# Kernel tuning notes

Hardware: AMD Instinct MI355X
Metric: run time of the kernel (lower is better)

## Reference

```python
import jax, jax.numpy as jnp
import numpy as np

D_IN = 768
D_OUT = 768
N_HEADS = 12
HEAD_DIM = D_OUT // N_HEADS


def setup_inputs() -> dict:
    key = jax.random.key(0)
    ks = jax.random.split(key, 6)
    B, S = 2, 4096
    x = jax.random.normal(ks[0], (B, S, D_IN), dtype=jnp.float32)
    s = 0.02
    Wq = jax.random.normal(ks[1], (D_IN, D_OUT), dtype=jnp.float32) * s
    Wk = jax.random.normal(ks[2], (D_IN, D_OUT), dtype=jnp.float32) * s
    Wv = jax.random.normal(ks[3], (D_IN, D_OUT), dtype=jnp.float32) * s
    Wo = jax.random.normal(ks[4], (D_OUT, D_OUT), dtype=jnp.float32) * s
    bo = jnp.zeros((D_OUT,), dtype=jnp.float32)
    return {"x": x, "Wq": Wq, "Wk": Wk, "Wv": Wv, "Wo": Wo, "bo": bo}


def reference(x, Wq, Wk, Wv, Wo, bo):
    B, S, _ = x.shape
    # QKV projections (no bias), reshape to [B, H, S, Dh]
    q = (x @ Wq).reshape(B, S, N_HEADS, HEAD_DIM).transpose(0, 2, 1, 3)
    k = (x @ Wk).reshape(B, S, N_HEADS, HEAD_DIM).transpose(0, 2, 1, 3)
    v = (x @ Wv).reshape(B, S, N_HEADS, HEAD_DIM).transpose(0, 2, 1, 3)
    # scores: [B, H, S, S], causal mask, scaled softmax
    scores = jnp.einsum('bhqd,bhkd->bhqk', q, k)
    causal = jnp.triu(jnp.ones((S, S), dtype=bool), k=1)
    scores = jnp.where(causal, -jnp.inf, scores)
    attn = jax.nn.softmax(scores / np.sqrt(HEAD_DIM).astype(np.float32), axis=-1)
    # dropout p=0.0 -> identity
    ctx = jnp.einsum('bhqk,bhkd->bqhd', attn, v).reshape(B, S, D_OUT)
    return ctx @ Wo + bo
```

## Files before the change

### kernel.cpp

```cpp
#include <hip/hip_runtime.h>

#define S 4096
#define BATCH 2
#define D 768
#define NH 12
#define DH 64
#define NROWS (BATCH * S)
#define N_ITEMS (32 * NH * BATCH)
#define CTR_OFF 67633152

typedef __attribute__((ext_vector_type(8))) short bf16x8;
typedef __attribute__((ext_vector_type(4))) float f32x4;
typedef __attribute__((ext_vector_type(2))) unsigned uint32x2;

__device__ __forceinline__ unsigned short f2bf(float f) {
    unsigned u = __builtin_bit_cast(unsigned, f);
    u += 0x7fff + ((u >> 16) & 1);
    return (unsigned short)(u >> 16);
}

__device__ __forceinline__ float fexp2(float x) {
#if __has_builtin(__builtin_amdgcn_exp2f)
    return __builtin_amdgcn_exp2f(x);
#else
    return exp2f(x);
#endif
}

#define GLDS16(g, l)                                                   \
    __builtin_amdgcn_global_load_lds(                                  \
        (const __attribute__((address_space(1))) void*)(g),            \
        (__attribute__((address_space(3))) void*)(l), 16, 0, 0)

__global__ __launch_bounds__(256) void cvt_x(const float* __restrict__ x,
                                             unsigned short* __restrict__ xb)
{
    int i = (blockIdx.x * 256 + threadIdx.x) * 4;
    float4 v = *(const float4*)(x + i);
    ushort4 o = make_ushort4(f2bf(v.x), f2bf(v.y), f2bf(v.z), f2bf(v.w));
    *(ushort4*)(xb + i) = o;
}

__global__ __launch_bounds__(256) void cvt_w(
    const float* __restrict__ Wq, const float* __restrict__ Wk,
    const float* __restrict__ Wv, const float* __restrict__ Wo,
    unsigned short* __restrict__ wt)
{
    __shared__ float tile[32][33];
    const int z = blockIdx.z;
    const float* W = (z == 0) ? Wq : (z == 1) ? Wk : (z == 2) ? Wv : Wo;
    const int k0 = blockIdx.x * 32, n0 = blockIdx.y * 32;
    const int t = threadIdx.x;
    const int r = t >> 3, c4 = (t & 7) * 4;

    float4 v = *(const float4*)(W + (size_t)(k0 + r) * D + n0 + c4);
    tile[r][c4 + 0] = v.x; tile[r][c4 + 1] = v.y;
    tile[r][c4 + 2] = v.z; tile[r][c4 + 3] = v.w;
    __syncthreads();
    ushort4 o = make_ushort4(f2bf(tile[c4 + 0][r]), f2bf(tile[c4 + 1][r]),
                             f2bf(tile[c4 + 2][r]), f2bf(tile[c4 + 3][r]));
    *(ushort4*)(wt + ((size_t)z * D + n0 + r) * D + k0 + c4) = o;
}

__global__ __launch_bounds__(256) void gemm_qkv(
    const unsigned short* __restrict__ xb,
    const unsigned short* __restrict__ wt,
    unsigned short* __restrict__ qb, unsigned short* __restrict__ kb,
    unsigned short* __restrict__ vtb)
{
    __shared__ unsigned short As[128 * 64];
    __shared__ unsigned short Bs[128 * 64];

    const int t = threadIdx.x;
    const int lane = t & 63, w = t >> 6;
    const int l16 = lane & 15, quad = lane >> 4;
    const int wm = w & 1, wn = w >> 1;
    const int m0 = blockIdx.x * 128;
    const int n0g = blockIdx.y * 128;
    const int z = n0g / 768;
    const int c0 = n0g - z * 768;
    const unsigned short* Wz = wt + (size_t)z * D * D;

    f32x4 acc[4][4] = {};

    for (int k0 = 0; k0 < D; k0 += 64) {
#pragma unroll
        for (int i = 0; i < 4; ++i) {
            int g = i * 256 + w * 64 + lane;
            int row = g >> 3, cl = g & 7, cg = cl ^ (row & 7);
            GLDS16(xb + (size_t)(m0 + row) * D + k0 + cg * 8,
                   As + (size_t)(i * 256 + w * 64) * 8);
            GLDS16(Wz + (size_t)(c0 + row) * D + k0 + cg * 8,
                   Bs + (size_t)(i * 256 + w * 64) * 8);
        }
        __syncthreads();
#pragma unroll
        for (int kk = 0; kk < 2; ++kk) {
            bf16x8 af[4], bf_[4];
#pragma unroll
            for (int mt = 0; mt < 4; ++mt) {
                int r = wm * 64 + mt * 16 + l16;
                int c = kk * 4 + quad;
                af[mt] = *(const bf16x8*)&As[(r * 8 + (c ^ (r & 7))) * 8];
            }
#pragma unroll
            for (int nt = 0; nt < 4; ++nt) {
                int r = wn * 64 + nt * 16 + l16;
                int c = kk * 4 + quad;
                bf_[nt] = *(const bf16x8*)&Bs[(r * 8 + (c ^ (r & 7))) * 8];
            }
#pragma unroll
            for (int mt = 0; mt < 4; ++mt)
#pragma unroll
                for (int nt = 0; nt < 4; ++nt)
                    acc[mt][nt] = __builtin_amdgcn_mfma_f32_16x16x32_bf16(
                        af[mt], bf_[nt], acc[mt][nt], 0, 0, 0);
        }
        __syncthreads();
    }

    if (z < 2) {
        unsigned short* outp = (z == 0) ? qb : kb;
        const float scale = (z == 0) ? 0.18033688011112042f : 1.0f;
#pragma unroll
        for (int mt = 0; mt < 4; ++mt) {
#pragma unroll
            for (int reg = 0; reg < 4; ++reg) {
                int m = wm * 64 + mt * 16 + quad * 4 + reg;
                int ng = m0 + m;
                int b = ng >> 12, s = ng & 4095;
#pragma unroll
                for (int nt = 0; nt < 4; ++nt) {
                    int n = c0 + wn * 64 + nt * 16 + l16;
                    int h = n >> 6, dh = n & 63;
                    outp[(((size_t)b * NH + h) * S + s) * DH + dh] =
                        f2bf(acc[mt][nt][reg] * scale);
                }
            }
        }
    } else {
#pragma unroll
        for (int mt = 0; mt < 4; ++mt) {
#pragma unroll
            for (int nt = 0; nt < 4; ++nt) {
                int m = wm * 64 + mt * 16 + quad * 4;
                int ng = m0 + m;
                int b = ng >> 12, s = ng & 4095;
                int n = c0 + wn * 64 + nt * 16 + l16;
                int h = n >> 6, dh = n & 63;
                ushort4 p = make_ushort4(
                    f2bf(acc[mt][nt][0]), f2bf(acc[mt][nt][1]),
                    f2bf(acc[mt][nt][2]), f2bf(acc[mt][nt][3]));
                *(ushort4*)(vtb + (((size_t)b * NH + h) * DH + dh) * S + s) = p;
            }
        }
    }
}

__global__ __launch_bounds__(256, 3) void attn_mfma(
    const unsigned short* __restrict__ qg,
    const unsigned short* __restrict__ kg,
    const unsigned short* __restrict__ vtg,
    unsigned short* __restrict__ ctxb,
    int* __restrict__ work_ctr)
{
    __shared__ unsigned short Ks[2][64 * 64];
    __shared__ unsigned short Vs[2][64 * 64];
    __shared__ int s_item;

    const float INF = __builtin_inff();
    const int t = threadIdx.x;
    const int w = t >> 6, lane = t & 63;
    const int l16 = lane & 15, quad = lane >> 4;
    const int a7 = l16 & 7;
    const int sg = w * 64 + lane;

    bf16x8 vone;
#pragma unroll
    for (int i = 0; i < 8; ++i) vone[i] = (short)0x3F80;

    for (;;) {
        if (t == 0) s_item = atomicAdd(work_ctr, 1);
        __syncthreads();
        const int p = s_item;
        if (p >= N_ITEMS) return;

        const int qt = 31 - (p / (NH * BATCH));
        const int hb = p % (NH * BATCH);
        const int h = hb % NH, b = hb / NH;
        const size_t hbase = ((size_t)b * NH + h) * (size_t)S * DH;
        const unsigned short* kp = kg + hbase;
        const unsigned short* vp = vtg + hbase;

        bf16x8 bq[2][2];
#pragma unroll
        for (int qs = 0; qs < 2; ++qs) {
            int qrow = qt * 128 + w * 32 + qs * 16 + l16;
#pragma unroll
            for (int kk = 0; kk < 2; ++kk)
                bq[qs][kk] = *(const bf16x8*)(qg + hbase + (size_t)qrow * DH +
                                              kk * 32 + quad * 8);
        }

        f32x4 acc_o[2][4] = {};
        f32x4 acc_sum[2] = {};

        const int jmax = 2 * qt + 1, jd = 2 * qt;

#pragma unroll
        for (int i = 0; i < 2; ++i) {
            int g = i * 256 + sg;
            int row = g >> 3, cl = g & 7, cg = cl ^ (row & 7);
            GLDS16(kp + (size_t)row * DH + cg * 8,
                   &Ks[0][(size_t)(i * 256 + w * 64) * 8]);
            GLDS16(vp + (size_t)row * S + cg * 8,
                   &Vs[0][(size_t)(i * 256 + w * 64) * 8]);
        }

        for (int j = 0; j <= jmax; ++j) {
            const int cur = j & 1;
            __syncthreads();
            if (j < jmax) {
#pragma unroll
                for (int i = 0; i < 2; ++i) {
                    int g = i * 256 + sg;
                    int row = g >> 3, cl = g & 7, cg = cl ^ (row & 7);
                    GLDS16(kp + (size_t)((j + 1) * 64 + row) * DH + cg * 8,
                           &Ks[cur ^ 1][(size_t)(i * 256 + w * 64) * 8]);
                    GLDS16(vp + (size_t)row * S + (j + 1) * 64 + cg * 8,
                           &Vs[cur ^ 1][(size_t)(i * 256 + w * 64) * 8]);
                }
            }

            const unsigned short* Kc = Ks[cur];
            const unsigned short* Vc = Vs[cur];

            f32x4 acc_s[2][4] = {};
            __builtin_amdgcn_s_setprio(1);
#pragma unroll
            for (int kk = 0; kk < 2; ++kk)
#pragma unroll
                for (int ms = 0; ms < 4; ++ms) {
                    int r = ms * 16 + l16, c = kk * 4 + quad;
                    bf16x8 ak = *(const bf16x8*)&Kc[(r * 8 + (c ^ a7)) * 8];
#pragma unroll
                    for (int qs = 0; qs < 2; ++qs)
                        acc_s[qs][ms] = __builtin_amdgcn_mfma_f32_16x16x32_bf16(
                            ak, bq[qs][kk], acc_s[qs][ms], 0, 0, 0);
                }
            __builtin_amdgcn_s_setprio(0);

            if (j >= jd) {
#pragma unroll
                for (int qs = 0; qs < 2; ++qs) {
                    int qrow_g = qt * 128 + w * 32 + qs * 16 + l16;
#pragma unroll
                    for (int ms = 0; ms < 4; ++ms)
#pragma unroll
                        for (int reg = 0; reg < 4; ++reg)
                            if ((j * 64 + ms * 16 + quad * 4 + reg) > qrow_g)
                                acc_s[qs][ms][reg] = -INF;
                }
            }

            bf16x8 bp[2][2];
#pragma unroll
            for (int qs = 0; qs < 2; ++qs) {
                unsigned ulo[4], uhi[4];
#pragma unroll
                for (int ms = 0; ms < 4; ++ms) {
                    float e0 = fexp2(acc_s[qs][ms][0]);
                    float e1 = fexp2(acc_s[qs][ms][1]);
                    float e2 = fexp2(acc_s[qs][ms][2]);
                    float e3 = fexp2(acc_s[qs][ms][3]);
                    asm("v_cvt_pk_bf16_f32 %0, %1, %2"
                        : "=v"(ulo[ms]) : "v"(e0), "v"(e1));
                    asm("v_cvt_pk_bf16_f32 %0, %1, %2"
                        : "=v"(uhi[ms]) : "v"(e2), "v"(e3));
                }
#pragma unroll
                for (int kp2 = 0; kp2 < 2; ++kp2) {
                    uint32x2 lo = __builtin_amdgcn_permlane32_swap(
                        ulo[2 * kp2], ulo[2 * kp2 + 1], false, false);
                    uint32x2 s02 = __builtin_amdgcn_permlane16_swap(
                        lo[0], lo[1], false, false);
                    uint32x2 hi = __builtin_amdgcn_permlane32_swap(
                        uhi[2 * kp2], uhi[2 * kp2 + 1], false, false);
                    uint32x2 s13 = __builtin_amdgcn_permlane16_swap(
                        hi[0], hi[1], false, false);
                    union { unsigned u[4]; bf16x8 v; } pb;
                    pb.u[0] = s02[0]; pb.u[1] = s13[0];
                    pb.u[2] = s02[1]; pb.u[3] = s13[1];
                    bp[qs][kp2] = pb.v;
                }
            }

            __builtin_amdgcn_s_setprio(1);
#pragma unroll
            for (int kk = 0; kk < 2; ++kk) {
#pragma unroll
                for (int d = 0; d < 4; ++d) {
                    int r = d * 16 + l16, c = kk * 4 + quad;
                    bf16x8 av = *(const bf16x8*)&Vc[(r * 8 + (c ^ a7)) * 8];
#pragma unroll
                    for (int qs = 0; qs < 2; ++qs)
                        acc_o[qs][d] = __builtin_amdgcn_mfma_f32_16x16x32_bf16(
                            av, bp[qs][kk], acc_o[qs][d], 0, 0, 0);
                }
#pragma unroll
                for (int qs = 0; qs < 2; ++qs)
                    acc_sum[qs] = __builtin_amdgcn_mfma_f32_16x16x32_bf16(
                        vone, bp[qs][kk], acc_sum[qs], 0, 0, 0);
            }
            __builtin_amdgcn_s_setprio(0);
        }

#pragma unroll
        for (int qs = 0; qs < 2; ++qs) {
            float inv = 1.f / acc_sum[qs][0];
            int qrow = qt * 128 + w * 32 + qs * 16 + l16;
            size_t base = ((size_t)(b * S + qrow)) * D + h * 64;
#pragma unroll
            for (int d = 0; d < 4; ++d) {
                ushort4 o;
                o.x = f2bf(acc_o[qs][d][0] * inv);
                o.y = f2bf(acc_o[qs][d][1] * inv);
                o.z = f2bf(acc_o[qs][d][2] * inv);
                o.w = f2bf(acc_o[qs][d][3] * inv);
                *(ushort4*)(ctxb + base + d * 16 + quad * 4) = o;
            }
        }
    }
}

__global__ __launch_bounds__(256) void gemm_out(
    const unsigned short* __restrict__ ctxb,
    const unsigned short* __restrict__ wt,
    const float* __restrict__ bo,
    float* __restrict__ out)
{
    __shared__ unsigned short As[128 * 64];
    __shared__ unsigned short Bs[128 * 64];

    const int t = threadIdx.x;
    const int lane = t & 63, w = t >> 6;
    const int l16 = lane & 15, quad = lane >> 4;
    const int wm = w & 1, wn = w >> 1;
    const int m0 = blockIdx.x * 128;
    const int n0 = blockIdx.y * 128;
    const unsigned short* Wz = wt + (size_t)3 * D * D;

    f32x4 acc[4][4] = {};

    for (int k0 = 0; k0 < D; k0 += 64) {
#pragma unroll
        for (int i = 0; i < 4; ++i) {
            int g = i * 256 + w * 64 + lane;
            int row = g >> 3, cl = g & 7, cg = cl ^ (row & 7);
            GLDS16(ctxb + (size_t)(m0 + row) * D + k0 + cg * 8,
                   As + (size_t)(i * 256 + w * 64) * 8);
            GLDS16(Wz + (size_t)(n0 + row) * D + k0 + cg * 8,
                   Bs + (size_t)(i * 256 + w * 64) * 8);
        }
        __syncthreads();
#pragma unroll
        for (int kk = 0; kk < 2; ++kk) {
            bf16x8 af[4], bf_[4];
#pragma unroll
            for (int mt = 0; mt < 4; ++mt) {
                int r = wm * 64 + mt * 16 + l16;
                int c = kk * 4 + quad;
                af[mt] = *(const bf16x8*)&As[(r * 8 + (c ^ (r & 7))) * 8];
            }
#pragma unroll
            for (int nt = 0; nt < 4; ++nt) {
                int r = wn * 64 + nt * 16 + l16;
                int c = kk * 4 + quad;
                bf_[nt] = *(const bf16x8*)&Bs[(r * 8 + (c ^ (r & 7))) * 8];
            }
#pragma unroll
            for (int mt = 0; mt < 4; ++mt)
#pragma unroll
                for (int nt = 0; nt < 4; ++nt)
                    acc[mt][nt] = __builtin_amdgcn_mfma_f32_16x16x32_bf16(
                        af[mt], bf_[nt], acc[mt][nt], 0, 0, 0);
        }
        __syncthreads();
    }

    float bv[4];
#pragma unroll
    for (int nt = 0; nt < 4; ++nt)
        bv[nt] = bo[n0 + wn * 64 + nt * 16 + l16];
#pragma unroll
    for (int mt = 0; mt < 4; ++mt)
#pragma unroll
        for (int reg = 0; reg < 4; ++reg) {
            int m = m0 + wm * 64 + mt * 16 + quad * 4 + reg;
#pragma unroll
            for (int nt = 0; nt < 4; ++nt)
                out[(size_t)m * D + n0 + wn * 64 + nt * 16 + l16] =
                    acc[mt][nt][reg] + bv[nt];
        }
}

extern "C" void kernel_launch(void* const* d_in, const int* in_sizes, int n_in,
                              void* d_out, int out_size, void* d_ws, size_t ws_size,
                              hipStream_t stream)
{
    const float* x  = (const float*)d_in[0];
    const float* Wq = (const float*)d_in[1];
    const float* Wk = (const float*)d_in[2];
    const float* Wv = (const float*)d_in[3];
    const float* Wo = (const float*)d_in[4];
    const float* bo = (const float*)d_in[5];
    float* out = (float*)d_out;

    const size_t elems = (size_t)NROWS * D;
    unsigned short* xb   = (unsigned short*)d_ws;
    unsigned short* wt   = xb + elems;
    unsigned short* q    = wt + (size_t)4 * D * D;
    unsigned short* k    = q + elems;
    unsigned short* vt   = k + elems;
    unsigned short* ctxb = vt + elems;
    int* work_ctr = (int*)((char*)d_ws + CTR_OFF);

    hipMemsetAsync(work_ctr, 0, sizeof(int), stream);

    cvt_x<<<NROWS * D / 1024, 256, 0, stream>>>(x, xb);
    dim3 gw(D / 32, D / 32, 4);
    cvt_w<<<gw, 256, 0, stream>>>(Wq, Wk, Wv, Wo, wt);

    dim3 g1(NROWS / 128, (3 * D) / 128);
    gemm_qkv<<<g1, 256, 0, stream>>>(xb, wt, q, k, vt);

    attn_mfma<<<512, 256, 0, stream>>>(q, k, vt, ctxb, work_ctr);

    dim3 g3(NROWS / 128, D / 128);
    gemm_out<<<g3, 256, 0, stream>>>(ctxb, wt, bo, out);
}
```

Baseline: 238.3 us.

## Software-pipeline QK^T of next tile with softmax/PV of current tile

```diff
diff --git a/kernel.cpp b/kernel.cpp
--- a/kernel.cpp
+++ b/kernel.cpp
@@ -157,6 +157,120 @@
     }
 }
 
+#define QK_CLUSTER(KSRC, DST)                                                \
+    {                                                                        \
+        _Pragma("unroll")                                                    \
+        for (int qs = 0; qs < 2; ++qs)                                       \
+            _Pragma("unroll")                                                \
+            for (int ms = 0; ms < 4; ++ms)                                   \
+                DST[qs][ms] = zf4;                                           \
+        __builtin_amdgcn_s_setprio(1);                                       \
+        _Pragma("unroll")                                                    \
+        for (int kk = 0; kk < 2; ++kk)                                       \
+            _Pragma("unroll")                                                \
+            for (int ms = 0; ms < 4; ++ms) {                                 \
+                int r = ms * 16 + l16, c = kk * 4 + quad;                    \
+                bf16x8 ak = *(const bf16x8*)&(KSRC)[(r * 8 + (c ^ a7)) * 8]; \
+                _Pragma("unroll")                                            \
+                for (int qs = 0; qs < 2; ++qs)                               \
+                    DST[qs][ms] = __builtin_amdgcn_mfma_f32_16x16x32_bf16(   \
+                        ak, bq[qs][kk], DST[qs][ms], 0, 0, 0);               \
+            }                                                                \
+        __builtin_amdgcn_s_setprio(0);                                       \
+    }
+
+#define PIPE_BODY(J, PAR, CUR, NXT)                                          \
+    {                                                                        \
+        const int j_ = (J);                                                  \
+        __builtin_amdgcn_sched_barrier(0);                                   \
+        __syncthreads();                                                     \
+        __builtin_amdgcn_sched_barrier(0);                                   \
+        if (j_ + 2 <= jmax) {                                                \
+            _Pragma("unroll")                                                \
+            for (int i = 0; i < 2; ++i) {                                    \
+                int g = i * 256 + sg;                                        \
+                int row = g >> 3, cg = (g & 7) ^ (row & 7);                  \
+                GLDS16(kp + (size_t)((j_ + 2) * 64 + row) * DH + cg * 8,     \
+                       &Ks[PAR][(size_t)(i * 256 + w * 64) * 8]);            \
+            }                                                                \
+        }                                                                    \
+        if (j_ + 1 <= jmax) {                                                \
+            _Pragma("unroll")                                                \
+            for (int i = 0; i < 2; ++i) {                                    \
+                int g = i * 256 + sg;                                        \
+                int row = g >> 3, cg = (g & 7) ^ (row & 7);                  \
+                GLDS16(vp + (size_t)row * S + (j_ + 1) * 64 + cg * 8,        \
+                       &Vs[(PAR) ^ 1][(size_t)(i * 256 + w * 64) * 8]);      \
+            }                                                                \
+        }                                                                    \
+        __builtin_amdgcn_sched_barrier(0);                                   \
+        if (j_ + 1 <= jmax) {                                                \
+            QK_CLUSTER(Ks[(PAR) ^ 1], NXT)                                   \
+        }                                                                    \
+        if (j_ >= jd) {                                                      \
+            _Pragma("unroll")                                                \
+            for (int qs = 0; qs < 2; ++qs) {                                 \
+                int qrow_g = qt * 128 + w * 32 + qs * 16 + l16;              \
+                _Pragma("unroll")                                            \
+                for (int ms = 0; ms < 4; ++ms)                               \
+                    _Pragma("unroll")                                        \
+                    for (int reg = 0; reg < 4; ++reg)                        \
+                        if ((j_ * 64 + ms * 16 + quad * 4 + reg) > qrow_g)   \
+                            CUR[qs][ms][reg] = -INF;                         \
+            }                                                                \
+        }                                                                    \
+        bf16x8 bp[2][2];                                                     \
+        _Pragma("unroll")                                                    \
+        for (int qs = 0; qs < 2; ++qs) {                                     \
+            unsigned ulo[4], uhi[4];                                         \
+            _Pragma("unroll")                                                \
+            for (int ms = 0; ms < 4; ++ms) {                                 \
+                float e0 = fexp2(CUR[qs][ms][0]);                            \
+                float e1 = fexp2(CUR[qs][ms][1]);                            \
+                float e2 = fexp2(CUR[qs][ms][2]);                            \
+                float e3 = fexp2(CUR[qs][ms][3]);                            \
+                asm("v_cvt_pk_bf16_f32 %0, %1, %2"                           \
+                    : "=v"(ulo[ms]) : "v"(e0), "v"(e1));                     \
+                asm("v_cvt_pk_bf16_f32 %0, %1, %2"                           \
+                    : "=v"(uhi[ms]) : "v"(e2), "v"(e3));                     \
+            }                                                                \
+            _Pragma("unroll")                                                \
+            for (int kp2 = 0; kp2 < 2; ++kp2) {                              \
+                uint32x2 lo = __builtin_amdgcn_permlane32_swap(              \
+                    ulo[2 * kp2], ulo[2 * kp2 + 1], false, false);           \
+                uint32x2 s02 = __builtin_amdgcn_permlane16_swap(             \
+                    lo[0], lo[1], false, false);                             \
+                uint32x2 hi = __builtin_amdgcn_permlane32_swap(              \
+                    uhi[2 * kp2], uhi[2 * kp2 + 1], false, false);           \
+                uint32x2 s13 = __builtin_amdgcn_permlane16_swap(             \
+                    hi[0], hi[1], false, false);                             \
+                union { unsigned u[4]; bf16x8 v; } pb;                       \
+                pb.u[0] = s02[0]; pb.u[1] = s13[0];                          \
+                pb.u[2] = s02[1]; pb.u[3] = s13[1];                          \
+                bp[qs][kp2] = pb.v;                                          \
+            }                                                                \
+        }                                                                    \
+        const unsigned short* Vc = Vs[PAR];                                  \
+        __builtin_amdgcn_s_setprio(1);                                       \
+        _Pragma("unroll")                                                    \
+        for (int kk = 0; kk < 2; ++kk) {                                     \
+            _Pragma("unroll")                                                \
+            for (int d = 0; d < 4; ++d) {                                    \
+                int r = d * 16 + l16, c = kk * 4 + quad;                     \
+                bf16x8 av = *(const bf16x8*)&Vc[(r * 8 + (c ^ a7)) * 8];     \
+                _Pragma("unroll")                                            \
+                for (int qs = 0; qs < 2; ++qs)                               \
+                    acc_o[qs][d] = __builtin_amdgcn_mfma_f32_16x16x32_bf16(  \
+                        av, bp[qs][kk], acc_o[qs][d], 0, 0, 0);              \
+            }                                                                \
+            _Pragma("unroll")                                                \
+            for (int qs = 0; qs < 2; ++qs)                                   \
+                acc_sum[qs] = __builtin_amdgcn_mfma_f32_16x16x32_bf16(       \
+                    vone, bp[qs][kk], acc_sum[qs], 0, 0, 0);                 \
+        }                                                                    \
+        __builtin_amdgcn_s_setprio(0);                                       \
+    }
+
 __global__ __launch_bounds__(256, 3) void attn_mfma(
     const unsigned short* __restrict__ qg,
     const unsigned short* __restrict__ kg,
@@ -169,6 +283,7 @@
     __shared__ int s_item;
 
     const float INF = __builtin_inff();
+    const f32x4 zf4 = {0.f, 0.f, 0.f, 0.f};
     const int t = threadIdx.x;
     const int w = t >> 6, lane = t & 63;
     const int l16 = lane & 15, quad = lane >> 4;
@@ -182,6 +297,7 @@
     for (;;) {
         if (t == 0) s_item = atomicAdd(work_ctr, 1);
         __syncthreads();
+        __builtin_amdgcn_sched_barrier(0);
         const int p = s_item;
         if (p >= N_ITEMS) return;
 
@@ -210,109 +326,24 @@
 #pragma unroll
         for (int i = 0; i < 2; ++i) {
             int g = i * 256 + sg;
-            int row = g >> 3, cl = g & 7, cg = cl ^ (row & 7);
+            int row = g >> 3, cg = (g & 7) ^ (row & 7);
             GLDS16(kp + (size_t)row * DH + cg * 8,
                    &Ks[0][(size_t)(i * 256 + w * 64) * 8]);
             GLDS16(vp + (size_t)row * S + cg * 8,
                    &Vs[0][(size_t)(i * 256 + w * 64) * 8]);
-        }
-
-        for (int j = 0; j <= jmax; ++j) {
-            const int cur = j & 1;
-            __syncthreads();
-            if (j < jmax) {
-#pragma unroll
-                for (int i = 0; i < 2; ++i) {
-                    int g = i * 256 + sg;
-                    int row = g >> 3, cl = g & 7, cg = cl ^ (row & 7);
-                    GLDS16(kp + (size_t)((j + 1) * 64 + row) * DH + cg * 8,
-                           &Ks[cur ^ 1][(size_t)(i * 256 + w * 64) * 8]);
-                    GLDS16(vp + (size_t)row * S + (j + 1) * 64 + cg * 8,
-                           &Vs[cur ^ 1][(size_t)(i * 256 + w * 64) * 8]);
-                }
-            }
-
-            const unsigned short* Kc = Ks[cur];
-            const unsigned short* Vc = Vs[cur];
-
-            f32x4 acc_s[2][4] = {};
-            __builtin_amdgcn_s_setprio(1);
-#pragma unroll
-            for (int kk = 0; kk < 2; ++kk)
-#pragma unroll
-                for (int ms = 0; ms < 4; ++ms) {
-                    int r = ms * 16 + l16, c = kk * 4 + quad;
-                    bf16x8 ak = *(const bf16x8*)&Kc[(r * 8 + (c ^ a7)) * 8];
-#pragma unroll
-                    for (int qs = 0; qs < 2; ++qs)
-                        acc_s[qs][ms] = __builtin_amdgcn_mfma_f32_16x16x32_bf16(
-                            ak, bq[qs][kk], acc_s[qs][ms], 0, 0, 0);
-                }
-            __builtin_amdgcn_s_setprio(0);
-
-            if (j >= jd) {
-#pragma unroll
-                for (int qs = 0; qs < 2; ++qs) {
-                    int qrow_g = qt * 128 + w * 32 + qs * 16 + l16;
-#pragma unroll
-                    for (int ms = 0; ms < 4; ++ms)
-#pragma unroll
-                        for (int reg = 0; reg < 4; ++reg)
-                            if ((j * 64 + ms * 16 + quad * 4 + reg) > qrow_g)
-                                acc_s[qs][ms][reg] = -INF;
-                }
-            }
-
-            bf16x8 bp[2][2];
-#pragma unroll
-            for (int qs = 0; qs < 2; ++qs) {
-                unsigned ulo[4], uhi[4];
-#pragma unroll
-                for (int ms = 0; ms < 4; ++ms) {
-                    float e0 = fexp2(acc_s[qs][ms][0]);
-                    float e1 = fexp2(acc_s[qs][ms][1]);
-                    float e2 = fexp2(acc_s[qs][ms][2]);
-                    float e3 = fexp2(acc_s[qs][ms][3]);
-                    asm("v_cvt_pk_bf16_f32 %0, %1, %2"
-                        : "=v"(ulo[ms]) : "v"(e0), "v"(e1));
-                    asm("v_cvt_pk_bf16_f32 %0, %1, %2"
-                        : "=v"(uhi[ms]) : "v"(e2), "v"(e3));
-                }
-#pragma unroll
-                for (int kp2 = 0; kp2 < 2; ++kp2) {
-                    uint32x2 lo = __builtin_amdgcn_permlane32_swap(
-                        ulo[2 * kp2], ulo[2 * kp2 + 1], false, false);
-                    uint32x2 s02 = __builtin_amdgcn_permlane16_swap(
-                        lo[0], lo[1], false, false);
-                    uint32x2 hi = __builtin_amdgcn_permlane32_swap(
-                        uhi[2 * kp2], uhi[2 * kp2 + 1], false, false);
-                    uint32x2 s13 = __builtin_amdgcn_permlane16_swap(
-                        hi[0], hi[1], false, false);
-                    union { unsigned u[4]; bf16x8 v; } pb;
-                    pb.u[0] = s02[0]; pb.u[1] = s13[0];
-                    pb.u[2] = s02[1]; pb.u[3] = s13[1];
-                    bp[qs][kp2] = pb.v;
-                }
-            }
-
-            __builtin_amdgcn_s_setprio(1);
-#pragma unroll
-            for (int kk = 0; kk < 2; ++kk) {
-#pragma unroll
-                for (int d = 0; d < 4; ++d) {
-                    int r = d * 16 + l16, c = kk * 4 + quad;
-                    bf16x8 av = *(const bf16x8*)&Vc[(r * 8 + (c ^ a7)) * 8];
-#pragma unroll
-                    for (int qs = 0; qs < 2; ++qs)
-                        acc_o[qs][d] = __builtin_amdgcn_mfma_f32_16x16x32_bf16(
-                            av, bp[qs][kk], acc_o[qs][d], 0, 0, 0);
-                }
-#pragma unroll
-                for (int qs = 0; qs < 2; ++qs)
-                    acc_sum[qs] = __builtin_amdgcn_mfma_f32_16x16x32_bf16(
-                        vone, bp[qs][kk], acc_sum[qs], 0, 0, 0);
-            }
-            __builtin_amdgcn_s_setprio(0);
+            GLDS16(kp + (size_t)(64 + row) * DH + cg * 8,
+                   &Ks[1][(size_t)(i * 256 + w * 64) * 8]);
+        }
+        __builtin_amdgcn_sched_barrier(0);
+        __syncthreads();
+        __builtin_amdgcn_sched_barrier(0);
+
+        f32x4 sA[2][4], sB[2][4];
+        QK_CLUSTER(Ks[0], sA)
+
+        for (int j = 0; j <= jmax; j += 2) {
+            PIPE_BODY(j, 0, sA, sB)
+            PIPE_BODY(j + 1, 1, sB, sA)
         }
 
 #pragma unroll
```

New measurement: 308.8 us. +29.6%, slower.

## Split attention work across 8 waves with 16 query rows each

Applied to the files above, without the earlier changes.

```diff
diff --git a/kernel.cpp b/kernel.cpp
--- a/kernel.cpp
+++ b/kernel.cpp
@@ -157,7 +157,7 @@
     }
 }
 
-__global__ __launch_bounds__(256, 3) void attn_mfma(
+__global__ __launch_bounds__(512, 4) void attn_mfma(
     const unsigned short* __restrict__ qg,
     const unsigned short* __restrict__ kg,
     const unsigned short* __restrict__ vtg,
@@ -173,7 +173,8 @@
     const int w = t >> 6, lane = t & 63;
     const int l16 = lane & 15, quad = lane >> 4;
     const int a7 = l16 & 7;
-    const int sg = w * 64 + lane;
+    const int srow = t >> 3;
+    const int scg = (t & 7) ^ (srow & 7);
 
     bf16x8 vone;
 #pragma unroll
@@ -192,50 +193,35 @@
         const unsigned short* kp = kg + hbase;
         const unsigned short* vp = vtg + hbase;
 
-        bf16x8 bq[2][2];
-#pragma unroll
-        for (int qs = 0; qs < 2; ++qs) {
-            int qrow = qt * 128 + w * 32 + qs * 16 + l16;
-#pragma unroll
-            for (int kk = 0; kk < 2; ++kk)
-                bq[qs][kk] = *(const bf16x8*)(qg + hbase + (size_t)qrow * DH +
-                                              kk * 32 + quad * 8);
-        }
-
-        f32x4 acc_o[2][4] = {};
-        f32x4 acc_sum[2] = {};
+        const int qrow = qt * 128 + w * 16 + l16;
+        bf16x8 bq[2];
+#pragma unroll
+        for (int kk = 0; kk < 2; ++kk)
+            bq[kk] = *(const bf16x8*)(qg + hbase + (size_t)qrow * DH +
+                                      kk * 32 + quad * 8);
+
+        f32x4 acc_o[4] = {};
+        f32x4 acc_sum = {};
 
         const int jmax = 2 * qt + 1, jd = 2 * qt;
 
-#pragma unroll
-        for (int i = 0; i < 2; ++i) {
-            int g = i * 256 + sg;
-            int row = g >> 3, cl = g & 7, cg = cl ^ (row & 7);
-            GLDS16(kp + (size_t)row * DH + cg * 8,
-                   &Ks[0][(size_t)(i * 256 + w * 64) * 8]);
-            GLDS16(vp + (size_t)row * S + cg * 8,
-                   &Vs[0][(size_t)(i * 256 + w * 64) * 8]);
-        }
+        GLDS16(kp + (size_t)srow * DH + scg * 8, &Ks[0][(size_t)w * 64 * 8]);
+        GLDS16(vp + (size_t)srow * S + scg * 8, &Vs[0][(size_t)w * 64 * 8]);
 
         for (int j = 0; j <= jmax; ++j) {
             const int cur = j & 1;
             __syncthreads();
             if (j < jmax) {
-#pragma unroll
-                for (int i = 0; i < 2; ++i) {
-                    int g = i * 256 + sg;
-                    int row = g >> 3, cl = g & 7, cg = cl ^ (row & 7);
-                    GLDS16(kp + (size_t)((j + 1) * 64 + row) * DH + cg * 8,
-                           &Ks[cur ^ 1][(size_t)(i * 256 + w * 64) * 8]);
-                    GLDS16(vp + (size_t)row * S + (j + 1) * 64 + cg * 8,
-                           &Vs[cur ^ 1][(size_t)(i * 256 + w * 64) * 8]);
-                }
+                GLDS16(kp + (size_t)((j + 1) * 64 + srow) * DH + scg * 8,
+                       &Ks[cur ^ 1][(size_t)w * 64 * 8]);
+                GLDS16(vp + (size_t)srow * S + (j + 1) * 64 + scg * 8,
+                       &Vs[cur ^ 1][(size_t)w * 64 * 8]);
             }
 
             const unsigned short* Kc = Ks[cur];
             const unsigned short* Vc = Vs[cur];
 
-            f32x4 acc_s[2][4] = {};
+            f32x4 acc_s[4] = {};
             __builtin_amdgcn_s_setprio(1);
 #pragma unroll
             for (int kk = 0; kk < 2; ++kk)
@@ -243,36 +229,29 @@
                 for (int ms = 0; ms < 4; ++ms) {
                     int r = ms * 16 + l16, c = kk * 4 + quad;
                     bf16x8 ak = *(const bf16x8*)&Kc[(r * 8 + (c ^ a7)) * 8];
-#pragma unroll
-                    for (int qs = 0; qs < 2; ++qs)
-                        acc_s[qs][ms] = __builtin_amdgcn_mfma_f32_16x16x32_bf16(
-                            ak, bq[qs][kk], acc_s[qs][ms], 0, 0, 0);
+                    acc_s[ms] = __builtin_amdgcn_mfma_f32_16x16x32_bf16(
+                        ak, bq[kk], acc_s[ms], 0, 0, 0);
                 }
             __builtin_amdgcn_s_setprio(0);
 
             if (j >= jd) {
 #pragma unroll
-                for (int qs = 0; qs < 2; ++qs) {
-                    int qrow_g = qt * 128 + w * 32 + qs * 16 + l16;
-#pragma unroll
-                    for (int ms = 0; ms < 4; ++ms)
-#pragma unroll
-                        for (int reg = 0; reg < 4; ++reg)
-                            if ((j * 64 + ms * 16 + quad * 4 + reg) > qrow_g)
-                                acc_s[qs][ms][reg] = -INF;
-                }
-            }
-
-            bf16x8 bp[2][2];
-#pragma unroll
-            for (int qs = 0; qs < 2; ++qs) {
+                for (int ms = 0; ms < 4; ++ms)
+#pragma unroll
+                    for (int reg = 0; reg < 4; ++reg)
+                        if ((j * 64 + ms * 16 + quad * 4 + reg) > qrow)
+                            acc_s[ms][reg] = -INF;
+            }
+
+            bf16x8 bp[2];
+            {
                 unsigned ulo[4], uhi[4];
 #pragma unroll
                 for (int ms = 0; ms < 4; ++ms) {
-                    float e0 = fexp2(acc_s[qs][ms][0]);
-                    float e1 = fexp2(acc_s[qs][ms][1]);
-                    float e2 = fexp2(acc_s[qs][ms][2]);
-                    float e3 = fexp2(acc_s[qs][ms][3]);
+                    float e0 = fexp2(acc_s[ms][0]);
+                    float e1 = fexp2(acc_s[ms][1]);
+                    float e2 = fexp2(acc_s[ms][2]);
+                    float e3 = fexp2(acc_s[ms][3]);
                     asm("v_cvt_pk_bf16_f32 %0, %1, %2"
                         : "=v"(ulo[ms]) : "v"(e0), "v"(e1));
                     asm("v_cvt_pk_bf16_f32 %0, %1, %2"
@@ -291,7 +270,7 @@
                     union { unsigned u[4]; bf16x8 v; } pb;
                     pb.u[0] = s02[0]; pb.u[1] = s13[0];
                     pb.u[2] = s02[1]; pb.u[3] = s13[1];
-                    bp[qs][kp2] = pb.v;
+                    bp[kp2] = pb.v;
                 }
             }
 
@@ -302,31 +281,25 @@
                 for (int d = 0; d < 4; ++d) {
                     int r = d * 16 + l16, c = kk * 4 + quad;
                     bf16x8 av = *(const bf16x8*)&Vc[(r * 8 + (c ^ a7)) * 8];
-#pragma unroll
-                    for (int qs = 0; qs < 2; ++qs)
-                        acc_o[qs][d] = __builtin_amdgcn_mfma_f32_16x16x32_bf16(
-                            av, bp[qs][kk], acc_o[qs][d], 0, 0, 0);
+                    acc_o[d] = __builtin_amdgcn_mfma_f32_16x16x32_bf16(
+                        av, bp[kk], acc_o[d], 0, 0, 0);
                 }
-#pragma unroll
-                for (int qs = 0; qs < 2; ++qs)
-                    acc_sum[qs] = __builtin_amdgcn_mfma_f32_16x16x32_bf16(
-                        vone, bp[qs][kk], acc_sum[qs], 0, 0, 0);
+                acc_sum = __builtin_amdgcn_mfma_f32_16x16x32_bf16(
+                    vone, bp[kk], acc_sum, 0, 0, 0);
             }
             __builtin_amdgcn_s_setprio(0);
         }
 
-#pragma unroll
-        for (int qs = 0; qs < 2; ++qs) {
-            float inv = 1.f / acc_sum[qs][0];
-            int qrow = qt * 128 + w * 32 + qs * 16 + l16;
+        {
+            float inv = 1.f / acc_sum[0];
             size_t base = ((size_t)(b * S + qrow)) * D + h * 64;
 #pragma unroll
             for (int d = 0; d < 4; ++d) {
                 ushort4 o;
-                o.x = f2bf(acc_o[qs][d][0] * inv);
-                o.y = f2bf(acc_o[qs][d][1] * inv);
-                o.z = f2bf(acc_o[qs][d][2] * inv);
-                o.w = f2bf(acc_o[qs][d][3] * inv);
+                o.x = f2bf(acc_o[d][0] * inv);
+                o.y = f2bf(acc_o[d][1] * inv);
+                o.z = f2bf(acc_o[d][2] * inv);
+                o.w = f2bf(acc_o[d][3] * inv);
                 *(ushort4*)(ctxb + base + d * 16 + quad * 4) = o;
             }
         }
@@ -434,7 +407,7 @@
     dim3 g1(NROWS / 128, (3 * D) / 128);
     gemm_qkv<<<g1, 256, 0, stream>>>(xb, wt, q, k, vt);
 
-    attn_mfma<<<512, 256, 0, stream>>>(q, k, vt, ctxb, work_ctr);
+    attn_mfma<<<512, 512, 0, stream>>>(q, k, vt, ctxb, work_ctr);
 
     dim3 g3(NROWS / 128, D / 128);
     gemm_out<<<g3, 256, 0, stream>>>(ctxb, wt, bo, out);
```

New measurement: 234.1 us. No clear change (-1.8%).
